# Kernel optimization log

Measured on AMD Instinct MI355X. Metric: run time of the kernel, lower is better.

The kernel has to match this reference:

```python
import jax, jax.numpy as jnp
import numpy as np

DIM_V, DIM_T, DIM_OUT, NUM_HEADS = 1024, 1024, 1024, 16
HEAD_DIM = DIM_OUT // NUM_HEADS
BETA = 1.0  # module multiplies scores by self.beta (=1); self.scale is unused


def setup_inputs() -> dict:
    key = jax.random.key(0)
    ks = jax.random.split(key, 12)
    B, N1, N2 = 8, 256, 4096
    E = jax.random.normal(ks[0], (B, N1, DIM_T), dtype=jnp.float32)
    I = jax.random.normal(ks[1], (B, N2, DIM_V), dtype=jnp.float32)
    s = 0.02
    # Conv1d(kernel_size=1) == linear; weights stored [out, in], bias [out]
    q_w = jax.random.normal(ks[2], (DIM_OUT, DIM_T), dtype=jnp.float32) * s
    q_b = jnp.zeros((DIM_OUT,), dtype=jnp.float32)
    k_w = jax.random.normal(ks[3], (DIM_OUT, DIM_V), dtype=jnp.float32) * s
    k_b = jnp.zeros((DIM_OUT,), dtype=jnp.float32)
    v_w = jax.random.normal(ks[4], (DIM_OUT, DIM_V), dtype=jnp.float32) * s
    v_b = jnp.zeros((DIM_OUT,), dtype=jnp.float32)
    p_w = jax.random.normal(ks[5], (DIM_OUT, DIM_OUT), dtype=jnp.float32) * s
    p_b = jnp.zeros((DIM_OUT,), dtype=jnp.float32)
    return {"E": E, "I": I, "q_w": q_w, "q_b": q_b, "k_w": k_w, "k_b": k_b,
            "v_w": v_w, "v_b": v_b, "p_w": p_w, "p_b": p_b}


def reference(E, I, q_w, q_b, k_w, k_b, v_w, v_b, p_w, p_b):
    B, N1, _ = E.shape
    _, N2, _ = I.shape
    # 1x1 conv projections == dense layers over channel dim
    Q = (jnp.einsum('bnc,oc->bno', E, q_w) + q_b).reshape(B, N1, NUM_HEADS, HEAD_DIM)
    K = (jnp.einsum('bmc,oc->bmo', I, k_w) + k_b).reshape(B, N2, NUM_HEADS, HEAD_DIM)
    V = (jnp.einsum('bmc,oc->bmo', I, v_w) + v_b).reshape(B, N2, NUM_HEADS, HEAD_DIM)
    # cross-attention scores [B, H, N1, N2]
    attn = jnp.einsum('bnhd,bmhd->bhnm', Q, K) * BETA
    attn = jax.nn.softmax(attn, axis=-1)
    U = jnp.einsum('bhnm,bmhd->bnhd', attn, V).reshape(B, N1, DIM_OUT)
    U = jnp.einsum('bnc,oc->bno', U, p_w) + p_b
    U = U / jnp.linalg.norm(U, axis=-1, keepdims=True)
    return jnp.concatenate([E, U], axis=2)  # [B, N1, dim_t + dim_out]
```

## Files before the change

kernel.cpp:

```cpp
#include <hip/hip_runtime.h>
#include <hip/hip_bf16.h>
#include <stdint.h>


typedef __bf16 bf16_t;
typedef __attribute__((ext_vector_type(8))) __bf16 bf16x8;
typedef __attribute__((ext_vector_type(4))) __bf16 bf16x4;
typedef __attribute__((ext_vector_type(4))) float f32x4;

#define DEVINL __device__ __forceinline__

DEVINL f32x4 mfma16(bf16x8 a, bf16x8 b, f32x4 c) {
  return __builtin_amdgcn_mfma_f32_16x16x32_bf16(a, b, c, 0, 0, 0);
}

DEVINL float fexp2(float x) { return __builtin_exp2f(x); }

DEVINL bf16x8 load8(const bf16_t* p) { return *(const bf16x8*)p; }
DEVINL bf16x8 load8(const float* p) {
  const float4 u = *(const float4*)p;
  const float4 v = *(const float4*)(p + 4);
  bf16x8 r;
  r[0] = (bf16_t)u.x; r[1] = (bf16_t)u.y; r[2] = (bf16_t)u.z; r[3] = (bf16_t)u.w;
  r[4] = (bf16_t)v.x; r[5] = (bf16_t)v.y; r[6] = (bf16_t)v.z; r[7] = (bf16_t)v.w;
  return r;
}

DEVINL uint32_t pack_bf16(float a, float b) {
  union { bf16_t h[2]; uint32_t u; } x;
  x.h[0] = (bf16_t)a; x.h[1] = (bf16_t)b;
  return x.u;
}

DEVINL void async16(const void* g, void* l) {
  typedef const __attribute__((address_space(1))) unsigned int* gp1;
  typedef __attribute__((address_space(3))) unsigned int* lp3;
  __builtin_amdgcn_global_load_lds((gp1)(uintptr_t)g,
                                   (lp3)(uint32_t)(uintptr_t)l, 16, 0, 0);
}

__global__ __launch_bounds__(256) void cvt_f32_bf16(
    const float* __restrict__ src, bf16_t* __restrict__ dst, int n8) {
  const int i = blockIdx.x * 256 + threadIdx.x;
  if (i < n8) *(bf16x8*)(dst + (size_t)i * 8) = load8(src + (size_t)i * 8);
}

template <int MODE>
__global__ __launch_bounds__(512, 2) void gemm_bt_async(
    const bf16_t* __restrict__ A, const bf16_t* __restrict__ B,
    const float* __restrict__ bias, bf16_t* __restrict__ C,
    int M, int N, int K) {
  __shared__ bf16_t As[2][256 * 64];
  __shared__ bf16_t Bs[2][256 * 64];
  const int tid = threadIdx.x;
  const int w = tid >> 6, lane = tid & 63, quad = lane >> 4, l16 = lane & 15;
  const int bid = blockIdx.x;
  const int swz = (bid & 7) * (int)(gridDim.x >> 3) + (bid >> 3);
  const int big = swz >> 2, small = swz & 3;
  const int bm = 256 * (MODE == 1 ? small : big);
  const int bn = 256 * (MODE == 1 ? big : small);
  const int wm = (w >> 2) * 128, wn = (w & 3) * 64;
  const int srow = tid >> 3;
  const int sc8 = ((tid & 7) ^ (srow & 7)) * 8;

  const bf16_t* Ag = A + (size_t)(bm + srow) * K + sc8;
  const bf16_t* Bg = B + (size_t)(bn + srow) * K + sc8;

  f32x4 acc[8][4] = {};

#define STAGE_TILE(buf, k0)                                                    \
  {                                                                            \
    _Pragma("unroll") for (int c = 0; c < 4; c++) {                            \
      async16(Ag + (size_t)(c * 64) * K + (k0), As[buf] + c * 4096 + tid * 8); \
      async16(Bg + (size_t)(c * 64) * K + (k0), Bs[buf] + c * 4096 + tid * 8); \
    }                                                                          \
  }

  STAGE_TILE(0, 0);
  int cur = 0;

  for (int k0 = 0; k0 < K; k0 += 64) {
    if (k0 + 64 < K) {
      STAGE_TILE(cur ^ 1, k0 + 64);
      asm volatile("s_waitcnt vmcnt(8)" ::: "memory");
    } else {
      asm volatile("s_waitcnt vmcnt(0)" ::: "memory");
    }
    __builtin_amdgcn_s_barrier();

#pragma unroll
    for (int ks = 0; ks < 2; ks++) {
      bf16x8 bfr[4];
#pragma unroll
      for (int nt = 0; nt < 4; nt++) {
        const int r = wn + nt * 16 + l16;
        bfr[nt] = *(const bf16x8*)(Bs[cur] + r * 64 +
                                   (((ks * 4 + quad) ^ (r & 7)) * 8));
      }
      __builtin_amdgcn_s_setprio(1);
#pragma unroll
      for (int mt = 0; mt < 8; mt++) {
        const int r = wm + mt * 16 + l16;
        const bf16x8 af = *(const bf16x8*)(As[cur] + r * 64 +
                                           (((ks * 4 + quad) ^ (r & 7)) * 8));
#pragma unroll
        for (int nt = 0; nt < 4; nt++)
          acc[mt][nt] = mfma16(af, bfr[nt], acc[mt][nt]);
      }
      __builtin_amdgcn_s_setprio(0);
    }
    asm volatile("s_waitcnt lgkmcnt(0)" ::: "memory");
    __builtin_amdgcn_s_barrier();
    cur ^= 1;
  }
#undef STAGE_TILE

#pragma unroll
  for (int mt = 0; mt < 8; mt++) {
#pragma unroll
    for (int nt = 0; nt < 4; nt++) {
      const int gm0 = bm + wm + mt * 16 + quad * 4;
      const int gn = bn + wn + nt * 16 + l16;
#pragma unroll
      for (int r = 0; r < 4; r++) {
        const int gm = gm0 + r;
        C[(size_t)gm * N + gn] =
            (bf16_t)(acc[mt][nt][r] + bias[MODE == 1 ? gm : gn]);
      }
    }
  }
}

template <int MODE, typename TA, typename TB>
__global__ __launch_bounds__(256) void gemm_bt_reg(
    const TA* __restrict__ A, const TB* __restrict__ B,
    const float* __restrict__ bias, void* __restrict__ Cv,
    int M, int N, int K) {
  __shared__ bf16_t As[128 * 32];
  __shared__ bf16_t Bs[128 * 32];
  const int tid = threadIdx.x;
  const int w = tid >> 6, lane = tid & 63, quad = lane >> 4, l16 = lane & 15;
  const int bm = blockIdx.x * 128, bn = blockIdx.y * 128;
  const int wm = (w & 1) * 64, wn = (w >> 1) * 64;
  const int srow = tid >> 2;
  const int swz = ((tid & 3) ^ (srow & 3)) * 8;

  const TA* Ag0 = A + (size_t)(bm + srow) * K + swz;
  const TA* Ag1 = Ag0 + (size_t)64 * K;
  const TB* Bg0 = B + (size_t)(bn + srow) * K + swz;
  const TB* Bg1 = Bg0 + (size_t)64 * K;
  bf16_t* Al0 = As + tid * 8;
  bf16_t* Al1 = As + 64 * 32 + tid * 8;
  bf16_t* Bl0 = Bs + tid * 8;
  bf16_t* Bl1 = Bs + 64 * 32 + tid * 8;

  f32x4 acc[4][4] = {};

  bf16x8 a0 = load8(Ag0), a1 = load8(Ag1);
  bf16x8 b0 = load8(Bg0), b1 = load8(Bg1);

  for (int k0 = 0; k0 < K; k0 += 32) {
    *(bf16x8*)Al0 = a0;
    *(bf16x8*)Al1 = a1;
    *(bf16x8*)Bl0 = b0;
    *(bf16x8*)Bl1 = b1;
    __syncthreads();
    if (k0 + 32 < K) {
      a0 = load8(Ag0 + k0 + 32);
      a1 = load8(Ag1 + k0 + 32);
      b0 = load8(Bg0 + k0 + 32);
      b1 = load8(Bg1 + k0 + 32);
    }
    bf16x8 af[4], bfr[4];
#pragma unroll
    for (int mt = 0; mt < 4; mt++) {
      const int r = wm + mt * 16 + l16;
      af[mt] = *(const bf16x8*)(As + r * 32 + ((quad ^ (r & 3)) * 8));
    }
#pragma unroll
    for (int nt = 0; nt < 4; nt++) {
      const int r = wn + nt * 16 + l16;
      bfr[nt] = *(const bf16x8*)(Bs + r * 32 + ((quad ^ (r & 3)) * 8));
    }
#pragma unroll
    for (int mt = 0; mt < 4; mt++)
#pragma unroll
      for (int nt = 0; nt < 4; nt++)
        acc[mt][nt] = mfma16(af[mt], bfr[nt], acc[mt][nt]);
    __syncthreads();
  }

#pragma unroll
  for (int mt = 0; mt < 4; mt++) {
#pragma unroll
    for (int nt = 0; nt < 4; nt++) {
      const int gm0 = bm + wm + mt * 16 + quad * 4;
      const int gn = bn + wn + nt * 16 + l16;
#pragma unroll
      for (int r = 0; r < 4; r++) {
        const int gm = gm0 + r;
        float v = acc[mt][nt][r] + bias[MODE == 1 ? gm : gn];
        if (MODE == 3) v *= 1.4426950408889634f;
        if (MODE == 2)
          ((float*)Cv)[(size_t)gm * N + gn] = v;
        else
          ((bf16_t*)Cv)[(size_t)gm * N + gn] = (bf16_t)v;
      }
    }
  }
}

DEVINL void attn_step2(bf16x8 ke0, bf16x8 ke1, bf16x8 ko0, bf16x8 ko1,
                       const bf16x8 (&vf)[4],
                       const bf16x8 (&qf0)[2], const bf16x8 (&qf1)[2],
                       f32x4 (&o)[4][2], float (&lacc)[2]) {
  const f32x4 cm44 = {-44.f, -44.f, -44.f, -44.f};
#pragma unroll
  for (int qg = 0; qg < 2; qg++) {
    f32x4 z0 = cm44;
    z0 = mfma16(ke0, qf0[qg], z0);
    const f32x4 ste = mfma16(ke1, qf1[qg], z0);
    f32x4 z1 = cm44;
    z1 = mfma16(ko0, qf0[qg], z1);
    const f32x4 sto = mfma16(ko1, qf1[qg], z1);
    const float pe0 = fexp2(ste[0]), pe1 = fexp2(ste[1]);
    const float pe2 = fexp2(ste[2]), pe3 = fexp2(ste[3]);
    const float po0 = fexp2(sto[0]), po1 = fexp2(sto[1]);
    const float po2 = fexp2(sto[2]), po3 = fexp2(sto[3]);
    lacc[qg] += ((pe0 + pe1) + (pe2 + pe3)) + ((po0 + po1) + (po2 + po3));
    union { uint32_t u[4]; bf16x8 v; } pb;
    pb.u[0] = pack_bf16(pe0, pe1);
    pb.u[1] = pack_bf16(pe2, pe3);
    pb.u[2] = pack_bf16(po0, po1);
    pb.u[3] = pack_bf16(po2, po3);
    o[0][qg] = mfma16(vf[0], pb.v, o[0][qg]);
    o[1][qg] = mfma16(vf[1], pb.v, o[1][qg]);
    o[2][qg] = mfma16(vf[2], pb.v, o[2][qg]);
    o[3][qg] = mfma16(vf[3], pb.v, o[3][qg]);
  }
}

__global__ __launch_bounds__(512, 4) void attn_regs(
    const bf16_t* __restrict__ QU, const bf16_t* __restrict__ Kbuf,
    const bf16_t* __restrict__ Vtbuf, float* __restrict__ opart,
    float* __restrict__ mls) {
  __shared__ __attribute__((aligned(16))) char smem[35840];
  bf16_t* Ks = (bf16_t*)smem;
  bf16_t* Vs = (bf16_t*)(smem + 16384);
  float* lo = (float*)smem;
  float* ll = (float*)(smem + 34816);
  const int tid = threadIdx.x;
  const int w = tid >> 6, lane = tid & 63, quad = lane >> 4, l16 = lane & 15;
  const int wq = w >> 1, wk = w & 1, xr = l16 & 7;
  const int flat = blockIdx.x;
  const int qt = flat >> 9, s = (flat >> 7) & 3, h = (flat >> 3) & 15, b = flat & 7;

  bf16x8 qf0[2], qf1[2];
  const bf16_t* qb =
      QU + (size_t)(b * 256 + qt * 128 + wq * 32 + l16) * 1024 + h * 64 + quad * 8;
#pragma unroll
  for (int qg = 0; qg < 2; qg++) {
    qf0[qg] = *(const bf16x8*)(qb + (size_t)qg * 16 * 1024);
    qf1[qg] = *(const bf16x8*)(qb + (size_t)qg * 16 * 1024 + 32);
  }

  const int krow = tid >> 3;
  const int ksc = (tid & 7) ^ (krow & 7);
  const int vrow = tid >> 4;
  const int vsc = (tid & 15) ^ (vrow & 7);
  const bf16_t* ksrc0 =
      Kbuf + (size_t)(b * 4096 + s * 1024 + krow) * 1024 + h * 64 + ksc * 8;
  const bf16_t* ksrc1 = ksrc0 + (size_t)64 * 1024;
  const bf16_t* vsrc0 =
      Vtbuf + (size_t)(h * 64 + vrow) * 32768 + b * 4096 + s * 1024 + vsc * 8;
  const bf16_t* vsrc1 = vsrc0 + (size_t)32 * 32768;

  f32x4 o[4][2] = {};
  float lacc[2] = {};

  for (int it = 0; it < 8; it++) {
    async16(ksrc0, Ks + tid * 8);
    async16(ksrc1, Ks + 4096 + tid * 8);
    async16(vsrc0, Vs + tid * 8);
    async16(vsrc1, Vs + 4096 + tid * 8);
    ksrc0 += (size_t)128 * 1024;
    ksrc1 += (size_t)128 * 1024;
    vsrc0 += 128;
    vsrc1 += 128;
    __syncthreads();
#pragma unroll
    for (int sub = 0; sub < 2; sub++) {
      const int rowe = wk * 64 + sub * 32 + l16, rowo = rowe + 16;
      const bf16x8 ke0 = *(const bf16x8*)(Ks + rowe * 64 + ((quad ^ xr) * 8));
      const bf16x8 ke1 =
          *(const bf16x8*)(Ks + rowe * 64 + (((quad + 4) ^ xr) * 8));
      const bf16x8 ko0 = *(const bf16x8*)(Ks + rowo * 64 + ((quad ^ xr) * 8));
      const bf16x8 ko1 =
          *(const bf16x8*)(Ks + rowo * 64 + (((quad + 4) ^ xr) * 8));
      bf16x8 vf[4];
      const int c8 = wk * 8 + sub * 4 + (quad >> 1), in4 = (quad & 1) * 4;
#pragma unroll
      for (int dt = 0; dt < 4; dt++) {
        const int vr = dt * 16 + l16;
        union { bf16x4 h4[2]; bf16x8 v; } u;
        u.h4[0] = *(const bf16x4*)(Vs + vr * 128 + ((c8 ^ xr) * 8) + in4);
        u.h4[1] =
            *(const bf16x4*)(Vs + vr * 128 + (((c8 + 2) ^ xr) * 8) + in4);
        vf[dt] = u.v;
      }
      attn_step2(ke0, ke1, ko0, ko1, vf, qf0, qf1, o, lacc);
    }
    __syncthreads();
  }

#pragma unroll
  for (int qg = 0; qg < 2; qg++) {
    lacc[qg] += __shfl_xor(lacc[qg], 16);
    lacc[qg] += __shfl_xor(lacc[qg], 32);
  }
  if (quad == 0) {
#pragma unroll
    for (int qg = 0; qg < 2; qg++) ll[wk * 128 + wq * 32 + qg * 16 + l16] = lacc[qg];
  }
  if (wk == 0) {
#pragma unroll
    for (int qg = 0; qg < 2; qg++)
#pragma unroll
      for (int dt = 0; dt < 4; dt++)
        *(f32x4*)&lo[(wq * 32 + qg * 16 + l16) * 68 + dt * 16 + quad * 4] =
            o[dt][qg];
  }
  __syncthreads();
  if (wk == 1) {
    const int pr0 = ((b * 16 + h) << 8) | (qt * 128 + wq * 32);
#pragma unroll
    for (int qg = 0; qg < 2; qg++) {
      const int q = wq * 32 + qg * 16 + l16;
      const int pr = pr0 + qg * 16 + l16;
#pragma unroll
      for (int dt = 0; dt < 4; dt++) {
        f32x4 t = *(const f32x4*)&lo[q * 68 + dt * 16 + quad * 4];
        t = t + o[dt][qg];
        *(f32x4*)(opart + ((size_t)s * 32768 + pr) * 64 + dt * 16 + quad * 4) = t;
      }
      if (quad == 0) mls[(size_t)s * 32768 + pr] = ll[q] + ll[128 + q];
    }
  }
}

__global__ __launch_bounds__(256) void attn_combine(
    const float* __restrict__ opart, const float* __restrict__ mls,
    bf16_t* __restrict__ QU) {
  const int w = threadIdx.x >> 6, lane = threadIdx.x & 63;
  const int pr = blockIdx.x * 4 + w;
  float L = 0.f, acc = 0.f;
#pragma unroll
  for (int s = 0; s < 4; s++) {
    L += mls[(size_t)s * 32768 + pr];
    acc += opart[((size_t)s * 32768 + pr) * 64 + lane];
  }
  const int b = pr >> 12, h = (pr >> 8) & 15, q = pr & 255;
  QU[(size_t)(b * 256 + q) * 1024 + h * 64 + lane] =
      (bf16_t)(acc / fmaxf(L, 1e-37f));
}

__global__ __launch_bounds__(256) void attn_old(
    bf16_t* QU, const bf16_t* __restrict__ Kbuf,
    const bf16_t* __restrict__ Vtbuf, int hg, int G, int Kst) {
  __shared__ bf16_t Ks[64 * 64];
  __shared__ bf16_t Vs[64 * 64];
  __shared__ bf16_t Ps[4][16 * 64];
  const int tid = threadIdx.x;
  const int w = tid >> 6, lane = tid & 63, quad = lane >> 4, l16 = lane & 15;
  const int flat = blockIdx.x;
  const int qt = flat / (8 * G);
  const int rem = flat - qt * 8 * G;
  const int hh = rem % G, b = rem / G;
  const int h = hg + hh;

  const int qrow = b * 256 + qt * 64 + w * 16 + l16;
  const bf16_t* qbase = QU + (size_t)qrow * 1024 + h * 64 + quad * 8;
  const bf16x8 qf0 = *(const bf16x8*)(qbase);
  const bf16x8 qf1 = *(const bf16x8*)(qbase + 32);

  const int srow = tid >> 3;
  const int swz = ((tid & 7) ^ (srow & 7)) * 8;
  const bf16_t* Kg = Kbuf + (size_t)(b * 4096 + srow) * Kst + hh * 64 + swz;
  const bf16_t* Vg = Vtbuf + (size_t)(hh * 64 + srow) * 32768 + b * 4096 + swz;

  f32x4 o[4] = {};
  float mrow[4] = {-1e30f, -1e30f, -1e30f, -1e30f};
  float lrow[4] = {0.f, 0.f, 0.f, 0.f};
  const float L2E = 1.4426950408889634f;

  bf16x8 kv0 = *(const bf16x8*)(Kg);
  bf16x8 kv1 = *(const bf16x8*)(Kg + (size_t)32 * Kst);
  bf16x8 vv0 = *(const bf16x8*)(Vg);
  bf16x8 vv1 = *(const bf16x8*)(Vg + (size_t)32 * 32768);

  for (int kt = 0; kt < 64; kt++) {
    __syncthreads();
    *(bf16x8*)(Ks + tid * 8) = kv0;
    *(bf16x8*)(Ks + 32 * 64 + tid * 8) = kv1;
    *(bf16x8*)(Vs + tid * 8) = vv0;
    *(bf16x8*)(Vs + 32 * 64 + tid * 8) = vv1;
    __syncthreads();
    if (kt < 63) {
      const size_t ko = (size_t)(kt + 1) * 64;
      kv0 = *(const bf16x8*)(Kg + ko * Kst);
      kv1 = *(const bf16x8*)(Kg + (ko + 32) * Kst);
      vv0 = *(const bf16x8*)(Vg + ko);
      vv1 = *(const bf16x8*)(Vg + ko + (size_t)32 * 32768);
    }

    f32x4 s[4];
#pragma unroll
    for (int nt = 0; nt < 4; nt++) {
      const int key = nt * 16 + l16;
      const bf16x8 kf0 = *(const bf16x8*)(Ks + key * 64 + ((quad ^ (key & 7)) * 8));
      const bf16x8 kf1 = *(const bf16x8*)(Ks + key * 64 + (((quad + 4) ^ (key & 7)) * 8));
      f32x4 z = {0.f, 0.f, 0.f, 0.f};
      z = mfma16(qf0, kf0, z);
      s[nt] = mfma16(qf1, kf1, z);
    }

    float mnew[4], alpha[4], rsum[4];
#pragma unroll
    for (int r = 0; r < 4; r++) {
      float mx = fmaxf(fmaxf(s[0][r], s[1][r]), fmaxf(s[2][r], s[3][r]));
      mx = fmaxf(mx, __shfl_xor(mx, 1));
      mx = fmaxf(mx, __shfl_xor(mx, 2));
      mx = fmaxf(mx, __shfl_xor(mx, 4));
      mx = fmaxf(mx, __shfl_xor(mx, 8));
      mnew[r] = fmaxf(mrow[r], mx);
      alpha[r] = exp2f((mrow[r] - mnew[r]) * L2E);
      rsum[r] = 0.f;
    }
#pragma unroll
    for (int nt = 0; nt < 4; nt++) {
      const int key = nt * 16 + l16;
#pragma unroll
      for (int r = 0; r < 4; r++) {
        const float p = exp2f((s[nt][r] - mnew[r]) * L2E);
        rsum[r] += p;
        const int q = quad * 4 + r;
        Ps[w][q * 64 + (((key >> 3) ^ (q & 7)) * 8) + (key & 7)] = (bf16_t)p;
      }
    }
#pragma unroll
    for (int r = 0; r < 4; r++) {
      rsum[r] += __shfl_xor(rsum[r], 1);
      rsum[r] += __shfl_xor(rsum[r], 2);
      rsum[r] += __shfl_xor(rsum[r], 4);
      rsum[r] += __shfl_xor(rsum[r], 8);
      lrow[r] = lrow[r] * alpha[r] + rsum[r];
      mrow[r] = mnew[r];
    }
#pragma unroll
    for (int nt = 0; nt < 4; nt++) {
      o[nt][0] *= alpha[0]; o[nt][1] *= alpha[1];
      o[nt][2] *= alpha[2]; o[nt][3] *= alpha[3];
    }

    __syncthreads();

    const bf16x8 pf0 = *(const bf16x8*)(&Ps[w][l16 * 64 + ((quad ^ (l16 & 7)) * 8)]);
    const bf16x8 pf1 = *(const bf16x8*)(&Ps[w][l16 * 64 + (((quad + 4) ^ (l16 & 7)) * 8)]);
#pragma unroll
    for (int nt = 0; nt < 4; nt++) {
      const int d = nt * 16 + l16;
      const bf16x8 vf0 = *(const bf16x8*)(Vs + d * 64 + ((quad ^ (d & 7)) * 8));
      const bf16x8 vf1 = *(const bf16x8*)(Vs + d * 64 + (((quad + 4) ^ (d & 7)) * 8));
      o[nt] = mfma16(pf0, vf0, o[nt]);
      o[nt] = mfma16(pf1, vf1, o[nt]);
    }
  }

  float inv[4];
#pragma unroll
  for (int r = 0; r < 4; r++) inv[r] = 1.0f / fmaxf(lrow[r], 1e-30f);
#pragma unroll
  for (int nt = 0; nt < 4; nt++) {
#pragma unroll
    for (int r = 0; r < 4; r++) {
      const int row = b * 256 + qt * 64 + w * 16 + quad * 4 + r;
      QU[(size_t)row * 1024 + h * 64 + nt * 16 + l16] = (bf16_t)(o[nt][r] * inv[r]);
    }
  }
}

__global__ __launch_bounds__(256) void norm_concat(
    const float* __restrict__ E, const float* __restrict__ P,
    float* __restrict__ out) {
  const int row = blockIdx.x, tid = threadIdx.x;
  const int w = tid >> 6, lane = tid & 63;

  *(float4*)(out + (size_t)row * 2048 + tid * 4) =
      *(const float4*)(E + (size_t)row * 1024 + tid * 4);

  const float4 p = *(const float4*)(P + (size_t)row * 1024 + tid * 4);
  float ss = p.x * p.x + p.y * p.y + p.z * p.z + p.w * p.w;
#pragma unroll
  for (int m = 1; m <= 32; m <<= 1) ss += __shfl_xor(ss, m);
  __shared__ float red[4];
  if (lane == 0) red[w] = ss;
  __syncthreads();
  const float rn = rsqrtf(fmaxf(red[0] + red[1] + red[2] + red[3], 1e-30f));
  float4 q;
  q.x = p.x * rn; q.y = p.y * rn; q.z = p.z * rn; q.w = p.w * rn;
  *(float4*)(out + (size_t)row * 2048 + 1024 + tid * 4) = q;
}

extern "C" void kernel_launch(void* const* d_in, const int* in_sizes, int n_in,
                              void* d_out, int out_size, void* d_ws, size_t ws_size,
                              hipStream_t stream) {
  (void)in_sizes; (void)n_in; (void)out_size;
  const float* E   = (const float*)d_in[0];
  const float* I   = (const float*)d_in[1];
  const float* q_w = (const float*)d_in[2];
  const float* q_b = (const float*)d_in[3];
  const float* k_w = (const float*)d_in[4];
  const float* k_b = (const float*)d_in[5];
  const float* v_w = (const float*)d_in[6];
  const float* v_b = (const float*)d_in[7];
  const float* p_w = (const float*)d_in[8];
  const float* p_b = (const float*)d_in[9];
  float* out = (float*)d_out;
  char* ws = (char*)d_ws;

  if (ws_size >= (200ull << 20)) {
    bf16_t* QU    = (bf16_t*)(ws);
    bf16_t* k_wbf = (bf16_t*)(ws + (4u << 20));
    bf16_t* v_wbf = (bf16_t*)(ws + (6u << 20));
    bf16_t* Ibf   = (bf16_t*)(ws + (8u << 20));
    float*  Pf    = (float*)(ws + (8u << 20));
    float*  opart = (float*)(ws + (16u << 20));
    float*  mls   = (float*)(ws + (52u << 20));
    bf16_t* Kbuf  = (bf16_t*)(ws + (72u << 20));
    bf16_t* Vtbuf = (bf16_t*)(ws + (136u << 20));

    cvt_f32_bf16<<<16384, 256, 0, stream>>>(I, Ibf, 32768 * 1024 / 8);
    cvt_f32_bf16<<<512, 256, 0, stream>>>(k_w, k_wbf, 1024 * 1024 / 8);
    cvt_f32_bf16<<<512, 256, 0, stream>>>(v_w, v_wbf, 1024 * 1024 / 8);

    gemm_bt_reg<3, float, float><<<dim3(16, 8), 256, 0, stream>>>(
        E, q_w, q_b, QU, 2048, 1024, 1024);
    gemm_bt_async<0><<<512, 512, 0, stream>>>(
        Ibf, k_wbf, k_b, Kbuf, 32768, 1024, 1024);
    gemm_bt_async<1><<<512, 512, 0, stream>>>(
        v_wbf, Ibf, v_b, Vtbuf, 1024, 32768, 1024);
    attn_regs<<<1024, 512, 0, stream>>>(QU, Kbuf, Vtbuf, opart, mls);
    attn_combine<<<8192, 256, 0, stream>>>(opart, mls, QU);
    gemm_bt_reg<2, bf16_t, float><<<dim3(16, 8), 256, 0, stream>>>(
        QU, p_w, p_b, Pf, 2048, 1024, 1024);
    norm_concat<<<2048, 256, 0, stream>>>(E, Pf, out);
  } else {
    int G = 2;
    if (ws_size >= (133ull << 20)) G = 16;
    else if (ws_size >= (69ull << 20)) G = 8;
    else if (ws_size >= (37ull << 20)) G = 4;
    bf16_t* QU    = (bf16_t*)(ws);
    bf16_t* Kbuf  = (bf16_t*)(ws + (4u << 20));
    bf16_t* Vtbuf = (bf16_t*)(ws + (4u << 20) + ((size_t)G << 22));
    float*  Pf    = (float*)(ws + (4u << 20));

    gemm_bt_reg<0, float, float><<<dim3(16, 8), 256, 0, stream>>>(
        E, q_w, q_b, QU, 2048, 1024, 1024);
    for (int hg = 0; hg < 16; hg += G) {
      const int Nh = G * 64;
      gemm_bt_reg<0, float, float><<<dim3(256, Nh / 128), 256, 0, stream>>>(
          I, k_w + (size_t)hg * 64 * 1024, k_b + hg * 64, Kbuf, 32768, Nh, 1024);
      gemm_bt_reg<1, float, float><<<dim3(Nh / 128, 256), 256, 0, stream>>>(
          v_w + (size_t)hg * 64 * 1024, I, v_b + hg * 64, Vtbuf, Nh, 32768, 1024);
      attn_old<<<32 * G, 256, 0, stream>>>(QU, Kbuf, Vtbuf, hg, G, Nh);
    }
    gemm_bt_reg<2, bf16_t, float><<<dim3(16, 8), 256, 0, stream>>>(
        QU, p_w, p_b, Pf, 2048, 1024, 1024);
    norm_concat<<<2048, 256, 0, stream>>>(E, Pf, out);
  }
}
```

Before: 540.6 us.

## Double-buffer attention K/V tiles and widen projection GEMM to 1024 threads

The attention kernel now prefetches the next K/V tile into a second LDS buffer while computing on the current one, replacing load-then-sync with a two-stage async pipeline. This hides global load latency but roughly doubles LDS use per block (66.5KB), which may reduce occupancy. The K/V projection GEMM goes from 512 to 1024 threads per block with 16 waves, each holding half as many accumulator tiles. This lowers register pressure and adds waves for latency hiding. The launch-bounds request of 4 blocks per CU is unlikely to be met given the 128KB LDS footprint per block.

Result: no change. 546.9 us (+1.2%).

```diff
diff --git a/kernel.cpp b/kernel.cpp
--- a/kernel.cpp
+++ b/kernel.cpp
@@ -46,7 +46,7 @@
 }
 
 template <int MODE>
-__global__ __launch_bounds__(512, 2) void gemm_bt_async(
+__global__ __launch_bounds__(1024, 4) void gemm_bt_async(
     const bf16_t* __restrict__ A, const bf16_t* __restrict__ B,
     const float* __restrict__ bias, bf16_t* __restrict__ C,
     int M, int N, int K) {
@@ -59,21 +59,21 @@
   const int big = swz >> 2, small = swz & 3;
   const int bm = 256 * (MODE == 1 ? small : big);
   const int bn = 256 * (MODE == 1 ? big : small);
-  const int wm = (w >> 2) * 128, wn = (w & 3) * 64;
+  const int wm = (w >> 2) * 64, wn = (w & 3) * 64;
   const int srow = tid >> 3;
   const int sc8 = ((tid & 7) ^ (srow & 7)) * 8;
 
   const bf16_t* Ag = A + (size_t)(bm + srow) * K + sc8;
   const bf16_t* Bg = B + (size_t)(bn + srow) * K + sc8;
 
-  f32x4 acc[8][4] = {};
-
-#define STAGE_TILE(buf, k0)                                                    \
-  {                                                                            \
-    _Pragma("unroll") for (int c = 0; c < 4; c++) {                            \
-      async16(Ag + (size_t)(c * 64) * K + (k0), As[buf] + c * 4096 + tid * 8); \
-      async16(Bg + (size_t)(c * 64) * K + (k0), Bs[buf] + c * 4096 + tid * 8); \
-    }                                                                          \
+  f32x4 acc[4][4] = {};
+
+#define STAGE_TILE(buf, k0)                                                     \
+  {                                                                             \
+    _Pragma("unroll") for (int c = 0; c < 2; c++) {                             \
+      async16(Ag + (size_t)(c * 128) * K + (k0), As[buf] + c * 8192 + tid * 8); \
+      async16(Bg + (size_t)(c * 128) * K + (k0), Bs[buf] + c * 8192 + tid * 8); \
+    }                                                                           \
   }
 
   STAGE_TILE(0, 0);
@@ -82,7 +82,7 @@
   for (int k0 = 0; k0 < K; k0 += 64) {
     if (k0 + 64 < K) {
       STAGE_TILE(cur ^ 1, k0 + 64);
-      asm volatile("s_waitcnt vmcnt(8)" ::: "memory");
+      asm volatile("s_waitcnt vmcnt(4)" ::: "memory");
     } else {
       asm volatile("s_waitcnt vmcnt(0)" ::: "memory");
     }
@@ -99,7 +99,7 @@
       }
       __builtin_amdgcn_s_setprio(1);
 #pragma unroll
-      for (int mt = 0; mt < 8; mt++) {
+      for (int mt = 0; mt < 4; mt++) {
         const int r = wm + mt * 16 + l16;
         const bf16x8 af = *(const bf16x8*)(As[cur] + r * 64 +
                                            (((ks * 4 + quad) ^ (r & 7)) * 8));
@@ -116,7 +116,7 @@
 #undef STAGE_TILE
 
 #pragma unroll
-  for (int mt = 0; mt < 8; mt++) {
+  for (int mt = 0; mt < 4; mt++) {
 #pragma unroll
     for (int nt = 0; nt < 4; nt++) {
       const int gm0 = bm + wm + mt * 16 + quad * 4;
@@ -244,11 +244,9 @@
     const bf16_t* __restrict__ QU, const bf16_t* __restrict__ Kbuf,
     const bf16_t* __restrict__ Vtbuf, float* __restrict__ opart,
     float* __restrict__ mls) {
-  __shared__ __attribute__((aligned(16))) char smem[35840];
-  bf16_t* Ks = (bf16_t*)smem;
-  bf16_t* Vs = (bf16_t*)(smem + 16384);
+  __shared__ __attribute__((aligned(16))) char smem[66560];
   float* lo = (float*)smem;
-  float* ll = (float*)(smem + 34816);
+  float* ll = (float*)(smem + 65536);
   const int tid = threadIdx.x;
   const int w = tid >> 6, lane = tid & 63, quad = lane >> 4, l16 = lane & 15;
   const int wq = w >> 1, wk = w & 1, xr = l16 & 7;
@@ -278,16 +276,33 @@
   f32x4 o[4][2] = {};
   float lacc[2] = {};
 
+#define ATTN_STAGE(bi)                                                   \
+  {                                                                      \
+    bf16_t* Ksb = (bf16_t*)(smem + (bi) * 16384);                        \
+    bf16_t* Vsb = (bf16_t*)(smem + 32768 + (bi) * 16384);                \
+    async16(ksrc0, Ksb + tid * 8);                                       \
+    async16(ksrc1, Ksb + 4096 + tid * 8);                                \
+    async16(vsrc0, Vsb + tid * 8);                                       \
+    async16(vsrc1, Vsb + 4096 + tid * 8);                                \
+    ksrc0 += (size_t)128 * 1024;                                         \
+    ksrc1 += (size_t)128 * 1024;                                         \
+    vsrc0 += 128;                                                        \
+    vsrc1 += 128;                                                        \
+  }
+
+  ATTN_STAGE(0);
+  int cur = 0;
+
   for (int it = 0; it < 8; it++) {
-    async16(ksrc0, Ks + tid * 8);
-    async16(ksrc1, Ks + 4096 + tid * 8);
-    async16(vsrc0, Vs + tid * 8);
-    async16(vsrc1, Vs + 4096 + tid * 8);
-    ksrc0 += (size_t)128 * 1024;
-    ksrc1 += (size_t)128 * 1024;
-    vsrc0 += 128;
-    vsrc1 += 128;
-    __syncthreads();
+    if (it < 7) {
+      ATTN_STAGE(cur ^ 1);
+      asm volatile("s_waitcnt vmcnt(4)" ::: "memory");
+    } else {
+      asm volatile("s_waitcnt vmcnt(0)" ::: "memory");
+    }
+    __builtin_amdgcn_s_barrier();
+    const bf16_t* Ks = (const bf16_t*)(smem + cur * 16384);
+    const bf16_t* Vs = (const bf16_t*)(smem + 32768 + cur * 16384);
 #pragma unroll
     for (int sub = 0; sub < 2; sub++) {
       const int rowe = wk * 64 + sub * 32 + l16, rowo = rowe + 16;
@@ -310,8 +325,11 @@
       }
       attn_step2(ke0, ke1, ko0, ko1, vf, qf0, qf1, o, lacc);
     }
-    __syncthreads();
-  }
+    asm volatile("s_waitcnt lgkmcnt(0)" ::: "memory");
+    __builtin_amdgcn_s_barrier();
+    cur ^= 1;
+  }
+#undef ATTN_STAGE
 
 #pragma unroll
   for (int qg = 0; qg < 2; qg++) {
@@ -545,9 +563,9 @@
 
     gemm_bt_reg<3, float, float><<<dim3(16, 8), 256, 0, stream>>>(
         E, q_w, q_b, QU, 2048, 1024, 1024);
-    gemm_bt_async<0><<<512, 512, 0, stream>>>(
+    gemm_bt_async<0><<<512, 1024, 0, stream>>>(
         Ibf, k_wbf, k_b, Kbuf, 32768, 1024, 1024);
-    gemm_bt_async<1><<<512, 512, 0, stream>>>(
+    gemm_bt_async<1><<<512, 1024, 0, stream>>>(
         v_wbf, Ibf, v_b, Vtbuf, 1024, 32768, 1024);
     attn_regs<<<1024, 512, 0, stream>>>(QU, Kbuf, Vtbuf, opart, mls);
     attn_combine<<<8192, 256, 0, stream>>>(opart, mls, QU);
```
